# Optimization experiments

Hardware: AMD Instinct MI355X
Metric: run time of the kernel (lower is better)

## Reference

```python
import jax, jax.numpy as jnp
import numpy as np

SHARPNESS_SIGMA = 0.75
EPS = 1e-17


def eps_denom(denom):
    # guard tiny denominators, preserving sign (sign of 0 treated as +1)
    sign = jnp.where(denom >= 0, 1.0, -1.0)
    return jnp.where(jnp.abs(denom) < EPS, sign * EPS, denom)


def setup_inputs() -> dict:
    key = jax.random.key(0)
    k1, k2 = jax.random.split(key)
    B, P, K = 4, 100000, 32
    normals = jax.random.normal(k1, (B, P, 3), dtype=jnp.float32)
    knn_idx = jax.random.randint(k2, (B, P, K), 0, P, dtype=jnp.int64)
    return {"normals": normals, "knn_idx": knn_idx}


def reference(normals, knn_idx):
    # knn_gather: [B,P,3] gathered at [B,P,K] -> [B,P,K,3]
    knn_normals = jax.vmap(lambda n, i: n[i])(normals, knn_idx)

    # get_normal_w: exp(-||n - ni||^2 / sigma^2) on unit normals
    inv_sigma = 1.0 / (SHARPNESS_SIGMA * SHARPNESS_SIGMA)
    n_unit = normals / eps_denom(jnp.linalg.norm(normals, axis=-1, keepdims=True))
    kn_unit = knn_normals / eps_denom(jnp.linalg.norm(knn_normals, axis=-1, keepdims=True))
    diff = kn_unit - n_unit[:, :, None, :]                      # [B,P,K,3]
    weights = jnp.exp(-jnp.sum(diff * diff, axis=-1) * inv_sigma)  # [B,P,K]

    # _denoise_normals: weighted average of (raw) neighbor normals
    num = jnp.sum(knn_normals * weights[:, :, :, None], axis=-2)   # [B,P,3]
    den = eps_denom(jnp.sum(weights, axis=-1, keepdims=True))      # [B,P,1]
    normals_denoised = num / den
    return normals_denoised
```

## Files before the change

kernel.cpp:

```cpp
#include <hip/hip_runtime.h>
#include <hip/hip_bf16.h>


#define SL_B 4
#define SL_P 100000
#define SL_K 32
#define SL_INV_SIG2 1.77777779f
#define SL_EPS 1e-17f

__global__ __launch_bounds__(256) void SurfaceLoss_kernel(
    const float* __restrict__ normals,
    const int*   __restrict__ knn,
    float*       __restrict__ out)
{
    int gid = blockIdx.x * blockDim.x + threadIdx.x;
    if (gid >= SL_B * SL_P) return;
    int b = gid / SL_P;

    const float* nb = normals + (size_t)b * SL_P * 3;

    float nx = normals[3 * (size_t)gid + 0];
    float ny = normals[3 * (size_t)gid + 1];
    float nz = normals[3 * (size_t)gid + 2];
    float nlen = sqrtf(nx * nx + ny * ny + nz * nz);
    float ninv = 1.0f / fmaxf(nlen, SL_EPS);
    float ux = nx * ninv, uy = ny * ninv, uz = nz * ninv;

    const int* kptr = knn + (size_t)gid * SL_K;

    float numx = 0.f, numy = 0.f, numz = 0.f, den = 0.f;

#pragma unroll
    for (int k0 = 0; k0 < SL_K; k0 += 4) {
        int4 i4 = *reinterpret_cast<const int4*>(kptr + k0);
        int idxs[4] = {i4.x, i4.y, i4.z, i4.w};
#pragma unroll
        for (int j = 0; j < 4; ++j) {
            int idx = idxs[j];
            float kx = nb[3 * (size_t)idx + 0];
            float ky = nb[3 * (size_t)idx + 1];
            float kz = nb[3 * (size_t)idx + 2];
            float klen = sqrtf(kx * kx + ky * ky + kz * kz);
            float kinv = 1.0f / fmaxf(klen, SL_EPS);
            float dx = kx * kinv - ux;
            float dy = ky * kinv - uy;
            float dz = kz * kinv - uz;
            float d2 = dx * dx + dy * dy + dz * dz;
            float w = __expf(-d2 * SL_INV_SIG2);
            numx = fmaf(kx, w, numx);
            numy = fmaf(ky, w, numy);
            numz = fmaf(kz, w, numz);
            den += w;
        }
    }

    float dinv = 1.0f / fmaxf(den, SL_EPS);
    out[3 * (size_t)gid + 0] = numx * dinv;
    out[3 * (size_t)gid + 1] = numy * dinv;
    out[3 * (size_t)gid + 2] = numz * dinv;
}

extern "C" void kernel_launch(void* const* d_in, const int* in_sizes, int n_in,
                              void* d_out, int out_size, void* d_ws, size_t ws_size,
                              hipStream_t stream) {
    const float* normals = (const float*)d_in[0];
    const int*   knn     = (const int*)d_in[1];
    float*       out     = (float*)d_out;

    int total = SL_B * SL_P;
    int block = 256;
    int grid = (total + block - 1) / block;
    SurfaceLoss_kernel<<<grid, block, 0, stream>>>(normals, knn, out);
}
```

Measured before the change: 69.22 us.

## Split neighbor loop across thread pairs and use float4 gathers

Each point is now handled by two threads, each processing half of the 32 neighbors, with partial sums combined by a lane shuffle. Neighbor normals are fetched with a single float4 load (shifted for the last element) instead of three scalar loads. This aims to raise memory-level parallelism and cut gather instruction count, at the cost of doubling thread count and slightly over-fetching bytes.

```diff
diff --git a/kernel.cpp b/kernel.cpp
--- a/kernel.cpp
+++ b/kernel.cpp
@@ -5,6 +5,7 @@
 #define SL_B 4
 #define SL_P 100000
 #define SL_K 32
+#define SL_HALF 16
 #define SL_INV_SIG2 1.77777779f
 #define SL_EPS 1e-17f
 
@@ -14,50 +15,70 @@
     float*       __restrict__ out)
 {
     int gid = blockIdx.x * blockDim.x + threadIdx.x;
-    if (gid >= SL_B * SL_P) return;
-    int b = gid / SL_P;
+    int p = gid >> 1;
+    if (p >= SL_B * SL_P) return;
+    int h = gid & 1;
+    int b = p / SL_P;
+    int pl = p - b * SL_P;
 
-    const float* nb = normals + (size_t)b * SL_P * 3;
+    const float* nb = normals + (size_t)b * (SL_P * 3);
 
-    float nx = normals[3 * (size_t)gid + 0];
-    float ny = normals[3 * (size_t)gid + 1];
-    float nz = normals[3 * (size_t)gid + 2];
-    float nlen = sqrtf(nx * nx + ny * ny + nz * nz);
-    float ninv = 1.0f / fmaxf(nlen, SL_EPS);
+    {
+    }
+    int coff = pl * 3;
+    bool clast = (pl == SL_P - 1);
+    float4 cv = *reinterpret_cast<const float4*>(nb + (clast ? coff - 1 : coff));
+    float nx = clast ? cv.y : cv.x;
+    float ny = clast ? cv.z : cv.y;
+    float nz = clast ? cv.w : cv.z;
+    float ninv = 1.0f / fmaxf(sqrtf(nx * nx + ny * ny + nz * nz), SL_EPS);
     float ux = nx * ninv, uy = ny * ninv, uz = nz * ninv;
 
-    const int* kptr = knn + (size_t)gid * SL_K;
+    int kid[SL_HALF];
+    const int4* kp = reinterpret_cast<const int4*>(knn + (size_t)p * SL_K + h * SL_HALF);
+#pragma unroll
+    for (int j = 0; j < 4; ++j) {
+        int4 q = kp[j];
+        kid[4 * j + 0] = q.x;
+        kid[4 * j + 1] = q.y;
+        kid[4 * j + 2] = q.z;
+        kid[4 * j + 3] = q.w;
+    }
 
     float numx = 0.f, numy = 0.f, numz = 0.f, den = 0.f;
 
 #pragma unroll
-    for (int k0 = 0; k0 < SL_K; k0 += 4) {
-        int4 i4 = *reinterpret_cast<const int4*>(kptr + k0);
-        int idxs[4] = {i4.x, i4.y, i4.z, i4.w};
-#pragma unroll
-        for (int j = 0; j < 4; ++j) {
-            int idx = idxs[j];
-            float kx = nb[3 * (size_t)idx + 0];
-            float ky = nb[3 * (size_t)idx + 1];
-            float kz = nb[3 * (size_t)idx + 2];
-            float klen = sqrtf(kx * kx + ky * ky + kz * kz);
-            float kinv = 1.0f / fmaxf(klen, SL_EPS);
-            float dx = kx * kinv - ux;
-            float dy = ky * kinv - uy;
-            float dz = kz * kinv - uz;
-            float d2 = dx * dx + dy * dy + dz * dz;
-            float w = __expf(-d2 * SL_INV_SIG2);
-            numx = fmaf(kx, w, numx);
-            numy = fmaf(ky, w, numy);
-            numz = fmaf(kz, w, numz);
-            den += w;
-        }
+    for (int k = 0; k < SL_HALF; ++k) {
+        int idx = kid[k];
+        int off = idx * 3;
+        bool last = (idx == SL_P - 1);
+        float4 v = *reinterpret_cast<const float4*>(nb + (last ? off - 1 : off));
+        float kx = last ? v.y : v.x;
+        float ky = last ? v.z : v.y;
+        float kz = last ? v.w : v.z;
+        float kinv = 1.0f / fmaxf(sqrtf(kx * kx + ky * ky + kz * kz), SL_EPS);
+        float dx = fmaf(kx, kinv, -ux);
+        float dy = fmaf(ky, kinv, -uy);
+        float dz = fmaf(kz, kinv, -uz);
+        float d2 = dx * dx + dy * dy + dz * dz;
+        float w = __expf(-d2 * SL_INV_SIG2);
+        numx = fmaf(kx, w, numx);
+        numy = fmaf(ky, w, numy);
+        numz = fmaf(kz, w, numz);
+        den += w;
     }
 
-    float dinv = 1.0f / fmaxf(den, SL_EPS);
-    out[3 * (size_t)gid + 0] = numx * dinv;
-    out[3 * (size_t)gid + 1] = numy * dinv;
-    out[3 * (size_t)gid + 2] = numz * dinv;
+    numx += __shfl_xor(numx, 1);
+    numy += __shfl_xor(numy, 1);
+    numz += __shfl_xor(numz, 1);
+    den  += __shfl_xor(den, 1);
+
+    if (h == 0) {
+        float dinv = 1.0f / fmaxf(den, SL_EPS);
+        out[3 * (size_t)p + 0] = numx * dinv;
+        out[3 * (size_t)p + 1] = numy * dinv;
+        out[3 * (size_t)p + 2] = numz * dinv;
+    }
 }
 
 extern "C" void kernel_launch(void* const* d_in, const int* in_sizes, int n_in,
@@ -67,7 +88,7 @@
     const int*   knn     = (const int*)d_in[1];
     float*       out     = (float*)d_out;
 
-    int total = SL_B * SL_P;
+    int total = SL_B * SL_P * 2;
     int block = 256;
     int grid = (total + block - 1) / block;
     SurfaceLoss_kernel<<<grid, block, 0, stream>>>(normals, knn, out);
```

New measurement: 71.49 us. 3.3% more time.
